# Optimization experiments

Measured on AMD Instinct MI355X. Metric: run time of the kernel, lower is better.

Reference implementation:

```python
import jax, jax.numpy as jnp
import numpy as np

B, C, K, P, H, W = 4, 128, 64, 8, 256, 256


def _img2patch(x, p):
    b, c, h, w = x.shape
    # [b,c,h,w] -> [b,c,p*p, (h//p)*(w//p)]
    return x.reshape(b, c, p, h // p, p, w // p).transpose(0, 1, 2, 4, 3, 5).reshape(b, c, p * p, -1)


def _patch2img(x, p, h, w):
    b, c = x.shape[:2]
    return x.reshape(b, c, p, p, h // p, w // p).transpose(0, 1, 2, 4, 3, 5).reshape(b, c, h, w)


def _conv1x1(x, Wm, bvec=None):
    # 1x1 conv on [b,c,pp,L] == channel matmul
    y = jnp.einsum('oc,bcpl->bopl', Wm, x)
    if bvec is not None:
        y = y + bvec[None, :, None, None]
    return y


def _l2norm(x, axis):
    return x / (1e-6 + jnp.sqrt(jnp.sum(x * x, axis=axis, keepdims=True)))


def setup_inputs():
    key = jax.random.key(0)
    ks = jax.random.split(key, 14)
    def wmat(k_, o, i):
        return jax.random.normal(k_, (o, i), jnp.float32) * np.float32(np.sqrt(2.0 / o))
    def bvec(k_, o):
        return jax.random.normal(k_, (o,), jnp.float32) * np.float32(0.01)
    return {
        'x1': jax.random.normal(ks[0], (B, C, H, W), jnp.float32),
        'x2': jax.random.normal(ks[1], (B, C, H, W), jnp.float32),
        'w_v': wmat(ks[2], K, 2 * C), 'b_v': bvec(ks[3], K),
        'w1_1': wmat(ks[4], C, C), 'b1_1': bvec(ks[5], C),
        'w2_1': wmat(ks[6], K, C), 'b2_1': bvec(ks[7], K),
        'w_out1': wmat(ks[8], C, C),
        'w1_2': wmat(ks[9], C, C), 'b1_2': bvec(ks[10], C),
        'w2_2': wmat(ks[11], K, C), 'b2_2': bvec(ks[12], K),
        'w_out2': wmat(ks[13], C, C),
        'p': P, 'k': K,
    }


def reference(x1, x2, w_v, b_v, w1_1, b1_1, w2_1, b2_1, w_out1, w1_2, b1_2, w2_2, b2_2, w_out2, p, k):
    b, c, h, w = x1.shape
    pp = p * p
    L = (h // p) * (w // p)
    bpp = b * pp
    x1p = _img2patch(x1, p)  # [b,c,pp,L]
    x2p = _img2patch(x2, p)
    y1_1 = _conv1x1(x1p, w1_1, b1_1).transpose(0, 2, 1, 3).reshape(bpp, c, L)
    y2_1 = _conv1x1(x1p, w2_1, b2_1).transpose(0, 2, 3, 1).reshape(bpp, L, k)
    y1_2 = _conv1x1(x2p, w1_2, b1_2).transpose(0, 2, 1, 3).reshape(bpp, c, L)
    y2_2 = _conv1x1(x2p, w2_2, b2_2).transpose(0, 2, 3, 1).reshape(bpp, L, k)
    v = _conv1x1(jnp.concatenate([x1p, x2p], axis=1), w_v, b_v)  # [b,k,pp,L]
    v = v.transpose(0, 2, 1, 3).reshape(bpp, k, L)
    v = jax.nn.softmax(v, axis=1)
    u1 = _l2norm(jnp.matmul(y1_1, y2_1), axis=1)  # [bpp,c,k]
    u2 = _l2norm(jnp.matmul(y1_2, y2_2), axis=1)
    y3_1 = jnp.matmul(u1, v).reshape(b, pp, c, L).transpose(0, 2, 1, 3)
    y3_2 = jnp.matmul(u2, v).reshape(b, pp, c, L).transpose(0, 2, 1, 3)
    out1 = jnp.einsum('oc,bchw->bohw', w_out1, _patch2img(y3_1, p, h, w))
    out2 = jnp.einsum('oc,bchw->bohw', w_out2, _patch2img(y3_2, p, h, w))
    return out1, out2
```

## Files before the change

kernel.cpp:

```cpp
#include <hip/hip_runtime.h>
#include <cstdint>

typedef __attribute__((ext_vector_type(8))) short short8;
typedef __attribute__((ext_vector_type(4))) float v4f;

#define B_ 4
#define C_ 128
#define K_ 64
#define H_ 256
#define W_ 256
#define HW_ (H_*W_)
#define L_ 1024
#define J_ 256
#define LC 128
#define NCH 8

#define OFF_WFH  0ull
#define OFF_WFL  131072ull
#define OFF_WOF  262144ull
#define OFF_BIAS 327680ull
#define OFF_VWS  335872ull

static __device__ __forceinline__ unsigned short f2bf(float x) {
    unsigned u = __builtin_bit_cast(unsigned, x);
    unsigned r = (u + 0x7FFFu + ((u >> 16) & 1u)) >> 16;
    return (unsigned short)r;
}
static __device__ __forceinline__ float bf2f(unsigned short h) {
    unsigned u = ((unsigned)h) << 16;
    return __builtin_bit_cast(float, u);
}
static __device__ __forceinline__ v4f mfma16(short8 a, short8 b, v4f c) {
    return __builtin_amdgcn_mfma_f32_16x16x32_bf16(a, b, c, 0, 0, 0);
}

union U8 { unsigned short u[8]; short8 v; };

__global__ void prep_kernel(const float* __restrict__ w_v, const float* __restrict__ b_v,
                            const float* __restrict__ w1_1, const float* __restrict__ b1_1,
                            const float* __restrict__ w2_1, const float* __restrict__ b2_1,
                            const float* __restrict__ wout1,
                            const float* __restrict__ w1_2, const float* __restrict__ b1_2,
                            const float* __restrict__ w2_2, const float* __restrict__ b2_2,
                            const float* __restrict__ wout2,
                            char* __restrict__ wsb) {
    int tid = blockIdx.x * 256 + threadIdx.x;
    if (tid < 65536) {
        int jj = tid & 7, lane = (tid >> 3) & 63, kc = (tid >> 9) & 3;
        int omt = (tid >> 11) & 15, s = (tid >> 15) & 1;
        int o = omt * 16 + (lane & 15);
        int c = kc * 32 + ((lane >> 4) * 8) + jj;
        const float* w1 = s ? w1_2 : w1_1;
        const float* w2 = s ? w2_2 : w2_1;
        float v;
        if (o < 128)      v = w1[o * 128 + c];
        else if (o < 192) v = w2[(o - 128) * 128 + c];
        else              v = w_v[(o - 192) * 256 + s * 128 + c];
        unsigned short hi = f2bf(v);
        unsigned short lo = f2bf(v - bf2f(hi));
        ((unsigned short*)(wsb + OFF_WFH))[tid] = hi;
        ((unsigned short*)(wsb + OFF_WFL))[tid] = lo;
    } else if (tid < 98304) {
        int id = tid - 65536;
        int jj = id & 7, lane = (id >> 3) & 63, kc = (id >> 9) & 3;
        int om = (id >> 11) & 7, s = (id >> 14) & 1;
        int o = om * 16 + (lane & 15);
        int c = kc * 32 + ((lane >> 4) * 8) + jj;
        const float* wo = s ? wout2 : wout1;
        ((unsigned short*)(wsb + OFF_WOF))[id] = f2bf(wo[o * 128 + c]);
    } else if (tid < 98816) {
        int id = tid - 98304;
        int s = id >> 8, o = id & 255;
        const float* b1 = s ? b1_2 : b1_1;
        const float* b2 = s ? b2_2 : b2_1;
        float v;
        if (o < 128)      v = b1[o];
        else if (o < 192) v = b2[o - 128];
        else              v = b_v[o - 192];
        ((float*)(wsb + OFF_BIAS))[id] = v;
    }
}

__global__ __attribute__((amdgpu_flat_work_group_size(512, 512), amdgpu_waves_per_eu(2, 2)))
void fused_kernel(
    const float* __restrict__ x1, const float* __restrict__ x2,
    char* __restrict__ wsb, float* __restrict__ out) {
    __shared__ __align__(16) char smem[151040];
    unsigned short* Xfh = (unsigned short*)&smem[0];
    unsigned short* Xfl = (unsigned short*)&smem[32768];
    unsigned short* Y1b = (unsigned short*)&smem[65536];
    unsigned short* Y2b = (unsigned short*)&smem[100352];
    float*          LG  = (float*)&smem[117760];
    float*          UF  = (float*)&smem[0];
    unsigned short* UH  = (unsigned short*)&smem[100352];
    unsigned short* MB  = (unsigned short*)&smem[65536];

    const unsigned short* wfh = (const unsigned short*)(wsb + OFF_WFH);
    const unsigned short* wfl = (const unsigned short*)(wsb + OFF_WFL);
    const unsigned short* wof = (const unsigned short*)(wsb + OFF_WOF);
    const float* biasws = (const float*)(wsb + OFF_BIAS);
    unsigned short* vws = (unsigned short*)(wsb + OFF_VWS);

    const int t = threadIdx.x;
    const int lane = t & 63;
    const int w = __builtin_amdgcn_readfirstlane(t >> 6);
    const int j = blockIdx.x;
    const int b = j >> 6, q = j & 63, i0 = q >> 3, i2 = q & 7;
    const long imgbase = (long)b * C_ * HW_ + (long)(i0 * 32) * W_ + i2 * 32;

    const int lquad = lane >> 4;
    const int lmod = lane & 15;

    float pb[2][2][4];
#pragma unroll
    for (int s = 0; s < 2; s++)
#pragma unroll
        for (int h = 0; h < 2; h++)
#pragma unroll
            for (int r = 0; r < 4; r++)
                pb[s][h][r] = biasws[s * 256 + w * 32 + h * 16 + lquad * 4 + r];

    v4f uacc[2][4];
#pragma unroll
    for (int s = 0; s < 2; s++)
#pragma unroll
        for (int kn = 0; kn < 4; kn++)
            uacc[s][kn] = (v4f){0.f, 0.f, 0.f, 0.f};

    const int dl = t & 127, c8 = t >> 7;
    const int srow = dl >> 5, scol = dl & 31;
    const int sln = dl >> 4, slp = dl & 15;

    float R[32];
#pragma unroll
    for (int p = 0; p < 4; p++)
#pragma unroll
        for (int jj = 0; jj < 8; jj++) {
            int c = (p * 4 + c8) * 8 + jj;
            R[p * 8 + jj] = x1[imgbase + (long)c * HW_ + srow * W_ + scol];
        }

    for (int lc = 0; lc < NCH; lc++) {
        v4f pacc[2][8];
#pragma unroll
        for (int s = 0; s < 2; s++) {
#pragma unroll
            for (int p = 0; p < 4; p++) {
                U8 hv, lv;
#pragma unroll
                for (int jj = 0; jj < 8; jj++) {
                    float v = R[p * 8 + jj];
                    unsigned short hh = f2bf(v);
                    hv.u[jj] = hh;
                    lv.u[jj] = f2bf(v - bf2f(hh));
                }
                int co = p * 4 + c8;
                int base = ((sln * 4 + (co >> 2)) * 64 + ((co & 3) * 16 + slp)) * 8;
                *(short8*)&Xfh[base] = hv.v;
                *(short8*)&Xfl[base] = lv.v;
            }
            __syncthreads();
            if (s == 0 || lc < NCH - 1) {
                const float* xp = s ? x1 : x2;
                const int nlc = s ? lc + 1 : lc;
#pragma unroll
                for (int p = 0; p < 4; p++)
#pragma unroll
                    for (int jj = 0; jj < 8; jj++) {
                        int c = (p * 4 + c8) * 8 + jj;
                        R[p * 8 + jj] = xp[imgbase + (long)c * HW_ + (nlc * 4 + srow) * W_ + scol];
                    }
            }
            if (s == 0 || w < 6) {
#pragma unroll
                for (int h = 0; h < 2; h++)
#pragma unroll
                    for (int ln = 0; ln < 8; ln++)
                        pacc[h][ln] = (v4f){pb[s][h][0], pb[s][h][1], pb[s][h][2], pb[s][h][3]};
            }
#pragma unroll
            for (int kc = 0; kc < 4; kc++) {
                int wi0 = (((s * 16 + (w * 2 + 0)) * 4 + kc) * 64 + lane) * 8;
                int wi1 = (((s * 16 + (w * 2 + 1)) * 4 + kc) * 64 + lane) * 8;
                short8 wh0 = *(const short8*)&wfh[wi0];
                short8 wh1 = *(const short8*)&wfh[wi1];
                short8 wlo0 = *(const short8*)&wfl[wi0];
                short8 wlo1 = *(const short8*)&wfl[wi1];
#pragma unroll
                for (int ln = 0; ln < 8; ln++) {
                    short8 bh = *(const short8*)&Xfh[((ln * 4 + kc) * 64 + lane) * 8];
                    short8 bl = *(const short8*)&Xfl[((ln * 4 + kc) * 64 + lane) * 8];
                    pacc[0][ln] = mfma16(wh0, bh, pacc[0][ln]);
                    pacc[0][ln] = mfma16(wlo0, bh, pacc[0][ln]);
                    pacc[0][ln] = mfma16(wh0, bl, pacc[0][ln]);
                    pacc[1][ln] = mfma16(wh1, bh, pacc[1][ln]);
                    pacc[1][ln] = mfma16(wlo1, bh, pacc[1][ln]);
                    pacc[1][ln] = mfma16(wh1, bl, pacc[1][ln]);
                }
            }
            if (w < 4) {
#pragma unroll
                for (int h = 0; h < 2; h++)
#pragma unroll
                    for (int ln = 0; ln < 8; ln++)
#pragma unroll
                        for (int r = 0; r < 4; r++)
                            Y1b[(w * 32 + h * 16 + lquad * 4 + r) * 136 + ln * 16 + lmod] = f2bf(pacc[h][ln][r]);
            } else if (w < 6) {
#pragma unroll
                for (int h = 0; h < 2; h++)
#pragma unroll
                    for (int ln = 0; ln < 8; ln++)
#pragma unroll
                        for (int r = 0; r < 4; r++)
                            Y2b[((w - 4) * 32 + h * 16 + lquad * 4 + r) * 136 + ln * 16 + lmod] = f2bf(pacc[h][ln][r]);
            } else if (s == 1) {
#pragma unroll
                for (int h = 0; h < 2; h++)
#pragma unroll
                    for (int ln = 0; ln < 8; ln++)
#pragma unroll
                        for (int r = 0; r < 4; r++)
                            LG[(ln * 16 + lmod) * 65 + (w - 6) * 32 + h * 16 + lquad * 4 + r] = pacc[h][ln][r];
            }
            __syncthreads();
#pragma unroll
            for (int kcl = 0; kcl < 4; kcl++) {
                short8 a = *(const short8*)&Y1b[(w * 16 + lmod) * 136 + kcl * 32 + lquad * 8];
#pragma unroll
                for (int kn = 0; kn < 4; kn++) {
                    short8 bb = *(const short8*)&Y2b[(kn * 16 + lmod) * 136 + kcl * 32 + lquad * 8];
                    uacc[s][kn] = mfma16(a, bb, uacc[s][kn]);
                }
            }
            if (s == 1) {
                int l2 = t >> 2, part = t & 3;
                float vv[16];
#pragma unroll
                for (int i = 0; i < 16; i++) vv[i] = LG[l2 * 65 + part * 16 + i];
                float mx = vv[0];
#pragma unroll
                for (int i = 1; i < 16; i++) mx = fmaxf(mx, vv[i]);
                mx = fmaxf(mx, __shfl_xor(mx, 1));
                mx = fmaxf(mx, __shfl_xor(mx, 2));
                float ssum = 0.f;
#pragma unroll
                for (int i = 0; i < 16; i++) { float e = __expf(vv[i] - mx); vv[i] = e; ssum += e; }
                ssum += __shfl_xor(ssum, 1);
                ssum += __shfl_xor(ssum, 2);
                float rs = 1.f / ssum;
                U8 o1, o2;
#pragma unroll
                for (int i = 0; i < 8; i++) o1.u[i] = f2bf(vv[i] * rs);
#pragma unroll
                for (int i = 0; i < 8; i++) o2.u[i] = f2bf(vv[8 + i] * rs);
                unsigned long long vb = ((unsigned long long)j * 1024 + lc * 128 + l2) * 64 + part * 16;
                *(short8*)&vws[vb] = o1.v;
                *(short8*)&vws[vb + 8] = o2.v;
            }
        }
    }

    __threadfence();

#pragma unroll
    for (int s = 0; s < 2; s++) {
        __syncthreads();
#pragma unroll
        for (int kn = 0; kn < 4; kn++)
#pragma unroll
            for (int r = 0; r < 4; r++)
                UF[(kn * 16 + lmod) * 133 + w * 16 + lquad * 4 + r] = uacc[s][kn][r];
        __syncthreads();
        if (t < 64) {
            const float* rp = &UF[t * 133];
            float ss = 0.f;
#pragma unroll 8
            for (int c = 0; c < 128; c++) ss += rp[c] * rp[c];
            UF[t * 133 + 128] = 1.f / (1e-6f + sqrtf(ss));
        }
        __syncthreads();
        {
            int kk = t >> 3, c0 = (t & 7) * 16;
            float rn = UF[kk * 133 + 128];
#pragma unroll
            for (int i = 0; i < 16; i++)
                UH[kk * 136 + c0 + i] = f2bf(UF[kk * 133 + c0 + i] * rn);
        }
        __syncthreads();
        v4f macc[4];
#pragma unroll
        for (int kn = 0; kn < 4; kn++) macc[kn] = (v4f){0.f, 0.f, 0.f, 0.f};
#pragma unroll
        for (int kc = 0; kc < 4; kc++) {
            short8 a = *(const short8*)&wof[(((s * 8 + w) * 4 + kc) * 64 + lane) * 8];
#pragma unroll
            for (int kn = 0; kn < 4; kn++) {
                short8 bb = *(const short8*)&UH[(kn * 16 + lmod) * 136 + kc * 32 + lquad * 8];
                macc[kn] = mfma16(a, bb, macc[kn]);
            }
        }
        __syncthreads();
#pragma unroll
        for (int kn = 0; kn < 4; kn++)
#pragma unroll
            for (int r = 0; r < 4; r++)
                MB[(w * 16 + lquad * 4 + r) * 72 + kn * 16 + lmod] = f2bf(macc[kn][r]);
        __syncthreads();
        short8 mfrag[2];
#pragma unroll
        for (int kc = 0; kc < 2; kc++)
            mfrag[kc] = *(const short8*)&MB[(w * 16 + lmod) * 72 + kc * 32 + lquad * 8];
        const long orow = (long)b * C_ * HW_ + (long)(i0 * 32) * W_ + i2 * 32
                        + (long)(w * 16 + lmod) * HW_ + (long)s * B_ * C_ * HW_;
#pragma unroll 4
        for (int ln = 0; ln < 64; ln++) {
            int l = ln * 16 + lmod;
            short8 b0  = *(const short8*)&vws[((unsigned long long)j * 1024 + l) * 64 + lquad * 8];
            short8 b1v = *(const short8*)&vws[((unsigned long long)j * 1024 + l) * 64 + 32 + lquad * 8];
            int lo = ln * 16 + lquad * 4;
            v4f acc = {0.f, 0.f, 0.f, 0.f};
            acc = mfma16(b0,  mfrag[0], acc);
            acc = mfma16(b1v, mfrag[1], acc);
            *(v4f*)&out[orow + (long)(lo >> 5) * W_ + (lo & 31)] = acc;
        }
    }
}

extern "C" void kernel_launch(void* const* d_in, const int* in_sizes, int n_in,
                              void* d_out, int out_size, void* d_ws, size_t ws_size,
                              hipStream_t stream) {
    (void)in_sizes; (void)n_in; (void)out_size; (void)ws_size;
    const float* x1    = (const float*)d_in[0];
    const float* x2    = (const float*)d_in[1];
    const float* w_v   = (const float*)d_in[2];
    const float* b_v   = (const float*)d_in[3];
    const float* w1_1  = (const float*)d_in[4];
    const float* b1_1  = (const float*)d_in[5];
    const float* w2_1  = (const float*)d_in[6];
    const float* b2_1  = (const float*)d_in[7];
    const float* wout1 = (const float*)d_in[8];
    const float* w1_2  = (const float*)d_in[9];
    const float* b1_2  = (const float*)d_in[10];
    const float* w2_2  = (const float*)d_in[11];
    const float* b2_2  = (const float*)d_in[12];
    const float* wout2 = (const float*)d_in[13];
    char* wsb  = (char*)d_ws;
    float* out = (float*)d_out;

    hipLaunchKernelGGL(prep_kernel, dim3(386), dim3(256), 0, stream,
                       w_v, b_v, w1_1, b1_1, w2_1, b2_1, wout1,
                       w1_2, b1_2, w2_2, b2_2, wout2, wsb);
    hipLaunchKernelGGL(fused_kernel, dim3(J_), dim3(512), 0, stream, x1, x2, wsb, out);
}
```

Baseline: 682.8 us.

## Split each patch across two blocks with atomic U reduction and last-block finalize

Each patch group is now handled by two workgroups, each covering half the rows, so the grid doubles from 256 to 512 blocks and per-block LDS use shrinks, allowing higher occupancy (waves_per_eu 4). The partial U accumulators are combined with float atomicAdd into a zeroed workspace. A per-patch counter then selects the second-arriving block to finish the normalization and output stage. This aims to fill more of the GPU's compute units, at the cost of atomic traffic, an extra zeroing pass in prep, and non-deterministic float summation order.

```diff
diff --git a/kernel.cpp b/kernel.cpp
--- a/kernel.cpp
+++ b/kernel.cpp
@@ -12,14 +12,15 @@
 #define HW_ (H_*W_)
 #define L_ 1024
 #define J_ 256
-#define LC 128
 #define NCH 8
 
 #define OFF_WFH  0ull
 #define OFF_WFL  131072ull
 #define OFF_WOF  262144ull
 #define OFF_BIAS 327680ull
+#define OFF_CTR  329728ull
 #define OFF_VWS  335872ull
+#define OFF_UWS  (OFF_VWS + 33554432ull)
 
 static __device__ __forceinline__ unsigned short f2bf(float x) {
     unsigned u = __builtin_bit_cast(unsigned, x);
@@ -78,33 +79,41 @@
         else if (o < 192) v = b2[o - 128];
         else              v = b_v[o - 192];
         ((float*)(wsb + OFF_BIAS))[id] = v;
+    } else if (tid < 99072) {
+        ((int*)(wsb + OFF_CTR))[tid - 98816] = 0;
     }
-}
-
-__global__ __attribute__((amdgpu_flat_work_group_size(512, 512), amdgpu_waves_per_eu(2, 2)))
+    float* uz = (float*)(wsb + OFF_UWS);
+    for (unsigned i = tid; i < 1048576u; i += 102400u)
+        *(v4f*)&uz[i * 4] = (v4f){0.f, 0.f, 0.f, 0.f};
+}
+
+__global__ __attribute__((amdgpu_flat_work_group_size(512, 512), amdgpu_waves_per_eu(4, 4)))
 void fused_kernel(
     const float* __restrict__ x1, const float* __restrict__ x2,
     char* __restrict__ wsb, float* __restrict__ out) {
-    __shared__ __align__(16) char smem[151040];
+    __shared__ __align__(16) char smem[77056];
     unsigned short* Xfh = (unsigned short*)&smem[0];
-    unsigned short* Xfl = (unsigned short*)&smem[32768];
-    unsigned short* Y1b = (unsigned short*)&smem[65536];
-    unsigned short* Y2b = (unsigned short*)&smem[100352];
-    float*          LG  = (float*)&smem[117760];
+    unsigned short* Xfl = (unsigned short*)&smem[16384];
+    unsigned short* Y1b = (unsigned short*)&smem[32768];
+    unsigned short* Y2b = (unsigned short*)&smem[51200];
+    float*          LG  = (float*)&smem[60416];
     float*          UF  = (float*)&smem[0];
-    unsigned short* UH  = (unsigned short*)&smem[100352];
-    unsigned short* MB  = (unsigned short*)&smem[65536];
+    unsigned short* UH  = (unsigned short*)&smem[51200];
+    unsigned short* MB  = (unsigned short*)&smem[0];
+    __shared__ int winflag;
 
     const unsigned short* wfh = (const unsigned short*)(wsb + OFF_WFH);
     const unsigned short* wfl = (const unsigned short*)(wsb + OFF_WFL);
     const unsigned short* wof = (const unsigned short*)(wsb + OFF_WOF);
     const float* biasws = (const float*)(wsb + OFF_BIAS);
     unsigned short* vws = (unsigned short*)(wsb + OFF_VWS);
+    float* Uws = (float*)(wsb + OFF_UWS);
 
     const int t = threadIdx.x;
     const int lane = t & 63;
     const int w = __builtin_amdgcn_readfirstlane(t >> 6);
-    const int j = blockIdx.x;
+    const int j = blockIdx.x & 255;
+    const int half = blockIdx.x >> 8;
     const int b = j >> 6, q = j & 63, i0 = q >> 3, i2 = q & 7;
     const long imgbase = (long)b * C_ * HW_ + (long)(i0 * 32) * W_ + i2 * 32;
 
@@ -127,25 +136,25 @@
         for (int kn = 0; kn < 4; kn++)
             uacc[s][kn] = (v4f){0.f, 0.f, 0.f, 0.f};
 
-    const int dl = t & 127, c8 = t >> 7;
-    const int srow = dl >> 5, scol = dl & 31;
-    const int sln = dl >> 4, slp = dl & 15;
-
-    float R[32];
-#pragma unroll
-    for (int p = 0; p < 4; p++)
+    const int ll = t & 63;
+    const int cw = t >> 6;
+    const int lgrp = ll >> 4, lp = ll & 15;
+
+    float R[16];
+#pragma unroll
+    for (int p = 0; p < 2; p++)
 #pragma unroll
         for (int jj = 0; jj < 8; jj++) {
-            int c = (p * 4 + c8) * 8 + jj;
-            R[p * 8 + jj] = x1[imgbase + (long)c * HW_ + srow * W_ + scol];
+            int c = (p * 8 + cw) * 8 + jj;
+            R[p * 8 + jj] = x1[imgbase + (long)c * HW_ + (half * 16 + (ll >> 5)) * W_ + (ll & 31)];
         }
 
     for (int lc = 0; lc < NCH; lc++) {
-        v4f pacc[2][8];
+        v4f pacc[2][4];
 #pragma unroll
         for (int s = 0; s < 2; s++) {
 #pragma unroll
-            for (int p = 0; p < 4; p++) {
+            for (int p = 0; p < 2; p++) {
                 U8 hv, lv;
 #pragma unroll
                 for (int jj = 0; jj < 8; jj++) {
@@ -154,28 +163,28 @@
                     hv.u[jj] = hh;
                     lv.u[jj] = f2bf(v - bf2f(hh));
                 }
-                int co = p * 4 + c8;
-                int base = ((sln * 4 + (co >> 2)) * 64 + ((co & 3) * 16 + slp)) * 8;
+                int co = p * 8 + cw;
+                int base = ((lgrp * 4 + (co >> 2)) * 64 + ((co & 3) * 16 + lp)) * 8;
                 *(short8*)&Xfh[base] = hv.v;
                 *(short8*)&Xfl[base] = lv.v;
             }
             __syncthreads();
             if (s == 0 || lc < NCH - 1) {
                 const float* xp = s ? x1 : x2;
-                const int nlc = s ? lc + 1 : lc;
-#pragma unroll
-                for (int p = 0; p < 4; p++)
+                const int nrow = half * 16 + (s ? (lc + 1) : lc) * 2 + (ll >> 5);
+#pragma unroll
+                for (int p = 0; p < 2; p++)
 #pragma unroll
                     for (int jj = 0; jj < 8; jj++) {
-                        int c = (p * 4 + c8) * 8 + jj;
-                        R[p * 8 + jj] = xp[imgbase + (long)c * HW_ + (nlc * 4 + srow) * W_ + scol];
+                        int c = (p * 8 + cw) * 8 + jj;
+                        R[p * 8 + jj] = xp[imgbase + (long)c * HW_ + (long)nrow * W_ + (ll & 31)];
                     }
             }
             if (s == 0 || w < 6) {
 #pragma unroll
                 for (int h = 0; h < 2; h++)
 #pragma unroll
-                    for (int ln = 0; ln < 8; ln++)
+                    for (int ln = 0; ln < 4; ln++)
                         pacc[h][ln] = (v4f){pb[s][h][0], pb[s][h][1], pb[s][h][2], pb[s][h][3]};
             }
 #pragma unroll
@@ -187,7 +196,7 @@
                 short8 wlo0 = *(const short8*)&wfl[wi0];
                 short8 wlo1 = *(const short8*)&wfl[wi1];
 #pragma unroll
-                for (int ln = 0; ln < 8; ln++) {
+                for (int ln = 0; ln < 4; ln++) {
                     short8 bh = *(const short8*)&Xfh[((ln * 4 + kc) * 64 + lane) * 8];
                     short8 bl = *(const short8*)&Xfl[((ln * 4 + kc) * 64 + lane) * 8];
                     pacc[0][ln] = mfma16(wh0, bh, pacc[0][ln]);
@@ -202,66 +211,88 @@
 #pragma unroll
                 for (int h = 0; h < 2; h++)
 #pragma unroll
-                    for (int ln = 0; ln < 8; ln++)
+                    for (int ln = 0; ln < 4; ln++)
 #pragma unroll
                         for (int r = 0; r < 4; r++)
-                            Y1b[(w * 32 + h * 16 + lquad * 4 + r) * 136 + ln * 16 + lmod] = f2bf(pacc[h][ln][r]);
+                            Y1b[(w * 32 + h * 16 + lquad * 4 + r) * 72 + ln * 16 + lmod] = f2bf(pacc[h][ln][r]);
             } else if (w < 6) {
 #pragma unroll
                 for (int h = 0; h < 2; h++)
 #pragma unroll
-                    for (int ln = 0; ln < 8; ln++)
+                    for (int ln = 0; ln < 4; ln++)
 #pragma unroll
                         for (int r = 0; r < 4; r++)
-                            Y2b[((w - 4) * 32 + h * 16 + lquad * 4 + r) * 136 + ln * 16 + lmod] = f2bf(pacc[h][ln][r]);
+                            Y2b[((w - 4) * 32 + h * 16 + lquad * 4 + r) * 72 + ln * 16 + lmod] = f2bf(pacc[h][ln][r]);
             } else if (s == 1) {
 #pragma unroll
                 for (int h = 0; h < 2; h++)
 #pragma unroll
-                    for (int ln = 0; ln < 8; ln++)
+                    for (int ln = 0; ln < 4; ln++)
 #pragma unroll
                         for (int r = 0; r < 4; r++)
                             LG[(ln * 16 + lmod) * 65 + (w - 6) * 32 + h * 16 + lquad * 4 + r] = pacc[h][ln][r];
             }
             __syncthreads();
 #pragma unroll
-            for (int kcl = 0; kcl < 4; kcl++) {
-                short8 a = *(const short8*)&Y1b[(w * 16 + lmod) * 136 + kcl * 32 + lquad * 8];
+            for (int kcl = 0; kcl < 2; kcl++) {
+                short8 a = *(const short8*)&Y1b[(w * 16 + lmod) * 72 + kcl * 32 + lquad * 8];
 #pragma unroll
                 for (int kn = 0; kn < 4; kn++) {
-                    short8 bb = *(const short8*)&Y2b[(kn * 16 + lmod) * 136 + kcl * 32 + lquad * 8];
+                    short8 bb = *(const short8*)&Y2b[(kn * 16 + lmod) * 72 + kcl * 32 + lquad * 8];
                     uacc[s][kn] = mfma16(a, bb, uacc[s][kn]);
                 }
             }
             if (s == 1) {
-                int l2 = t >> 2, part = t & 3;
-                float vv[16];
-#pragma unroll
-                for (int i = 0; i < 16; i++) vv[i] = LG[l2 * 65 + part * 16 + i];
+                int l2 = t >> 3, part = t & 7;
+                float vv[8];
+#pragma unroll
+                for (int i = 0; i < 8; i++) vv[i] = LG[l2 * 65 + part * 8 + i];
                 float mx = vv[0];
 #pragma unroll
-                for (int i = 1; i < 16; i++) mx = fmaxf(mx, vv[i]);
+                for (int i = 1; i < 8; i++) mx = fmaxf(mx, vv[i]);
                 mx = fmaxf(mx, __shfl_xor(mx, 1));
                 mx = fmaxf(mx, __shfl_xor(mx, 2));
+                mx = fmaxf(mx, __shfl_xor(mx, 4));
                 float ssum = 0.f;
 #pragma unroll
-                for (int i = 0; i < 16; i++) { float e = __expf(vv[i] - mx); vv[i] = e; ssum += e; }
+                for (int i = 0; i < 8; i++) { float e = __expf(vv[i] - mx); vv[i] = e; ssum += e; }
                 ssum += __shfl_xor(ssum, 1);
                 ssum += __shfl_xor(ssum, 2);
+                ssum += __shfl_xor(ssum, 4);
                 float rs = 1.f / ssum;
-                U8 o1, o2;
+                U8 o1;
 #pragma unroll
                 for (int i = 0; i < 8; i++) o1.u[i] = f2bf(vv[i] * rs);
-#pragma unroll
-                for (int i = 0; i < 8; i++) o2.u[i] = f2bf(vv[8 + i] * rs);
-                unsigned long long vb = ((unsigned long long)j * 1024 + lc * 128 + l2) * 64 + part * 16;
+                unsigned long long vb = ((unsigned long long)j * 1024 + half * 512 + lc * 64 + l2) * 64 + part * 8;
                 *(short8*)&vws[vb] = o1.v;
-                *(short8*)&vws[vb + 8] = o2.v;
             }
         }
     }
 
+    {
+        float* up = &Uws[(unsigned)j * 16384u];
+#pragma unroll
+        for (int s = 0; s < 2; s++)
+#pragma unroll
+            for (int kn = 0; kn < 4; kn++) {
+                int base = (((s * 8 + w) * 4 + kn) * 64 + lane) * 4;
+#pragma unroll
+                for (int r = 0; r < 4; r++)
+                    atomicAdd(&up[base + r], uacc[s][kn][r]);
+            }
+    }
     __threadfence();
+    __syncthreads();
+    if (t == 0) winflag = atomicAdd((int*)(wsb + OFF_CTR) + j, 1);
+    __syncthreads();
+    if (winflag == 0) return;
+    __threadfence();
+
+#pragma unroll
+    for (int s = 0; s < 2; s++)
+#pragma unroll
+        for (int kn = 0; kn < 4; kn++)
+            uacc[s][kn] = *(const v4f*)&Uws[(unsigned)j * 16384u + (((s * 8 + w) * 4 + kn) * 64 + lane) * 4];
 
 #pragma unroll
     for (int s = 0; s < 2; s++) {
@@ -348,8 +379,8 @@
     char* wsb  = (char*)d_ws;
     float* out = (float*)d_out;
 
-    hipLaunchKernelGGL(prep_kernel, dim3(386), dim3(256), 0, stream,
+    hipLaunchKernelGGL(prep_kernel, dim3(400), dim3(256), 0, stream,
                        w_v, b_v, w1_1, b1_1, w2_1, b2_1, wout1,
                        w1_2, b1_2, w2_2, b2_2, wout2, wsb);
-    hipLaunchKernelGGL(fused_kernel, dim3(J_), dim3(512), 0, stream, x1, x2, wsb, out);
-}
+    hipLaunchKernelGGL(fused_kernel, dim3(512), dim3(512), 0, stream, x1, x2, wsb, out);
+}
```

New measurement: 1.067 ms. 1.56x slower.
